# Kernel optimization log

Hardware: AMD Instinct MI355X
Metric: run time of the kernel (lower is better)

The kernel has to match this reference:

```python
import jax, jax.numpy as jnp
import numpy as np

B, L, D = 32, 1024, 1024
H = 8            # hard-coded in FourierBlock weights1 leading dim
E = D // H       # 128
M = 64           # number of retained low-frequency modes
K = 25           # moving_avg kernel (stride 1)
PAD = (K - 1) // 2


def setup_inputs() -> dict:
    key = jax.random.key(0)
    ks = jax.random.split(key, 7)
    scale = 1.0 / (D * D)
    return {
        "x":   jax.random.normal(ks[0], (B, L, D), jnp.float32),
        "Wq":  jax.random.normal(ks[1], (D, D), jnp.float32) * 0.02,
        "bq":  jax.random.normal(ks[2], (D,), jnp.float32) * 0.02,
        "w1r": jax.random.uniform(ks[3], (H, E, E, M), jnp.float32) * scale,
        "w1i": jax.random.uniform(ks[4], (H, E, E, M), jnp.float32) * scale,
        "Wo":  jax.random.normal(ks[5], (D, D), jnp.float32) * 0.02,
        "bo":  jax.random.normal(ks[6], (D,), jnp.float32) * 0.02,
    }


def _forward(x, Wq, bq, w1r, w1i, Wo, bo):
    # --- AutoCorrelationLayer query projection (k,v projections are dead code in FourierBlock) ---
    q = (x @ Wq + bq).reshape(B, L, H, E)          # [B,L,H,E]
    # --- FourierBlock ---
    xq = q.transpose(0, 2, 3, 1)                   # [B,H,E,L]
    x_ft = jnp.fft.rfft(xq, axis=-1)               # [B,H,E,F], F=L//2+1, complex64
    w = w1r + 1j * w1i                             # [H,E,E,M]
    # mode_select='low': index = [0..M-1], output slot wi == i
    out_sel = jnp.einsum("bhem,heom->bhom", x_ft[..., :M], w)   # [B,H,E,M]
    F = L // 2 + 1
    out_ft = jnp.zeros((B, H, E, F), dtype=x_ft.dtype).at[..., :M].set(out_sel)
    y = jnp.fft.irfft(out_ft, n=L, axis=-1)        # [B,H,E,L] real
    # faithful to torch: .view(B, L, -1) on contiguous (B,H,E,L) = flat C-order reshape
    out = y.reshape(B, L, H * E)
    new_x = out @ Wo + bo                          # out_projection
    x2 = x + new_x                                 # dropout is identity in eval
    # --- series_decomp (moving average k=25, replicate padding, stride 1) ---
    xp = jnp.concatenate(
        [jnp.repeat(x2[:, :1], PAD, axis=1), x2, jnp.repeat(x2[:, -1:], PAD, axis=1)],
        axis=1)                                    # [B, L+2*PAD, D]
    cs = jnp.cumsum(xp, axis=1)
    cs = jnp.concatenate([jnp.zeros_like(cs[:, :1]), cs], axis=1)
    moving_mean = (cs[:, K:] - cs[:, :-K]) / K     # [B,L,D]
    res = x2 - moving_mean
    return res


def reference(x, Wq, bq, w1r, w1i, Wo, bo):
    # module returns (x, attn) with attn=None; we return the array output
    return _forward(x, Wq, bq, w1r, w1i, Wo, bo)
```

## Files before the change

kernel.cpp:

```cpp
#include <hip/hip_runtime.h>
#include <hip/hip_bf16.h>

typedef __bf16 bf16x8 __attribute__((ext_vector_type(8)));
typedef float f32x4 __attribute__((ext_vector_type(4)));
typedef unsigned short u16;
typedef unsigned int u32;
typedef unsigned long long u64;


static __device__ __forceinline__ u16 f2b(float f) {
  u32 u = __builtin_bit_cast(u32, f);
  u32 r = (u + 0x7FFFu + ((u >> 16) & 1u)) >> 16;
  return (u16)r;
}
static __device__ __forceinline__ float b2f(u16 s) {
  u32 u = ((u32)s) << 16;
  return __builtin_bit_cast(float, u);
}
static __device__ __forceinline__ u32 pk2(float lo, float hi) {
  return (u32)f2b(lo) | ((u32)f2b(hi) << 16);
}
static __device__ __forceinline__ f32x4 mfma16(bf16x8 a, bf16x8 b, f32x4 c) {
  return __builtin_amdgcn_mfma_f32_16x16x32_bf16(a, b, c, 0, 0, 0);
}

__global__ __launch_bounds__(256) void k_prep(
    const float* __restrict__ Wq, const float* __restrict__ Wo,
    u16* __restrict__ FT, u16* __restrict__ FI2,
    u16* __restrict__ Wq16, u16* __restrict__ Wo16) {
  int idx = blockIdx.x * 256 + threadIdx.x;
  const float W0 = 6.283185307179586f / 1024.0f;
  if (idx < 131072) {
    int m2 = idx >> 10, l = idx & 1023;
    int m = (m2 < 64) ? m2 : (m2 - 64);
    int t = (m * l) & 1023;
    float s, c;
    __sincosf((float)t * W0, &s, &c);
    FT[idx] = f2b((m2 < 64) ? c : -s);
  } else if (idx < 262144) {
    int jj = idx - 131072;
    int j = jj >> 10, l = jj & 1023;
    int m = j >> 1;
    int t = (m * l) & 1023;
    float s, c;
    __sincosf((float)t * W0, &s, &c);
    float v;
    if ((j & 1) == 0) v = (m == 0) ? (1.0f / 1024.0f) : c * (2.0f / 1024.0f);
    else              v = (m == 0) ? 0.0f : -s * (2.0f / 1024.0f);
    FI2[jj] = f2b(v);
  } else if (idx < 262144 + 1048576) {
    int k = idx - 262144;
    Wq16[k] = f2b(Wq[k]);
  } else {
    int k = idx - 1310720;
    Wo16[k] = f2b(Wo[k]);
  }
}

__global__ __launch_bounds__(256) void k_wtrans(
    const float* __restrict__ w1r, const float* __restrict__ w1i,
    u16* __restrict__ W2r, u16* __restrict__ W2i) {
  __shared__ float T[128 * 65];
  int h = blockIdx.x >> 7, e = blockIdx.x & 127;
  int tid = threadIdx.x;
  for (int pass = 0; pass < 2; ++pass) {
    const float* src = pass ? w1i : w1r;
    u16* dst = pass ? W2i : W2r;
    {
      int m = tid & 63, og = tid >> 6;
      const float* sp = src + (((size_t)h * 128 + e) * 128) * 64 + m;
      for (int k = 0; k < 32; ++k) {
        int o = og * 32 + k;
        T[o * 65 + m] = sp[(size_t)o * 64];
      }
    }
    __syncthreads();
    {
      int o = tid & 127, mg = tid >> 7;
      for (int k = 0; k < 32; ++k) {
        int m = mg * 32 + k;
        dst[(((size_t)h * 64 + m) * 128 + e) * 128 + o] = f2b(T[o * 65 + m]);
      }
    }
    __syncthreads();
  }
}

template <int KSTEPS, bool BIAS>
static __device__ __forceinline__ void gemm128(
    const u16* __restrict__ A, size_t arow0, int astride,
    const u16* __restrict__ Bm, int bcol0,
    u16* __restrict__ C, size_t crow0, const float* __restrict__ bias) {
  __shared__ __align__(16) u16 Al[128 * 40];
  __shared__ __align__(16) u16 Bl[128 * 40];
  int tid = threadIdx.x, lane = tid & 63, w = tid >> 6;
  f32x4 acc[2][8];
#pragma unroll
  for (int i = 0; i < 2; i++)
#pragma unroll
    for (int j = 0; j < 8; j++) acc[i][j] = (f32x4){0.f, 0.f, 0.f, 0.f};
  int ar = tid >> 1, ahalf = tid & 1;
  int dloc = tid & 127, lg = tid >> 7;
  for (int kk = 0; kk < KSTEPS; ++kk) {
    {
      const uint4* src = (const uint4*)(A + (arow0 + ar) * (size_t)astride + kk * 32 + ahalf * 16);
      uint4 v0 = src[0], v1 = src[1];
      uint4* dst = (uint4*)(Al + ar * 40 + ahalf * 16);
      dst[0] = v0; dst[1] = v1;
    }
    {
#pragma unroll
      for (int jj = 0; jj < 4; ++jj) {
        int l0 = lg * 16 + jj * 4;
        const u16* bp = Bm + (size_t)(kk * 32 + l0) * 1024 + bcol0 + dloc;
        u16 s0 = bp[0], s1 = bp[1024], s2 = bp[2048], s3 = bp[3072];
        *(u64*)(Bl + dloc * 40 + l0) =
            (u64)s0 | ((u64)s1 << 16) | ((u64)s2 << 32) | ((u64)s3 << 48);
      }
    }
    __syncthreads();
    bf16x8 af[2];
#pragma unroll
    for (int mi = 0; mi < 2; mi++)
      af[mi] = *(const bf16x8*)(Al + (w * 32 + mi * 16 + (lane & 15)) * 40 + 8 * (lane >> 4));
#pragma unroll
    for (int ni = 0; ni < 8; ni++) {
      bf16x8 bf = *(const bf16x8*)(Bl + (ni * 16 + (lane & 15)) * 40 + 8 * (lane >> 4));
#pragma unroll
      for (int mi = 0; mi < 2; mi++) acc[mi][ni] = mfma16(af[mi], bf, acc[mi][ni]);
    }
    __syncthreads();
  }
  if (BIAS) {
    if (w == 0 && (lane >> 4) == 0) {
#pragma unroll
      for (int ni = 0; ni < 8; ni++)
        acc[0][ni][0] += 1024.0f * bias[bcol0 + ni * 16 + (lane & 15)];
    }
  }
#pragma unroll
  for (int mi = 0; mi < 2; mi++)
#pragma unroll
    for (int ni = 0; ni < 8; ni++)
#pragma unroll
      for (int r = 0; r < 4; r++) {
        int row = w * 32 + mi * 16 + 4 * (lane >> 4) + r;
        int col = bcol0 + ni * 16 + (lane & 15);
        C[(crow0 + row) * (size_t)1024 + col] = f2b(acc[mi][ni][r]);
      }
}

__global__ __launch_bounds__(256) void k_dft(const float* __restrict__ x,
                                             const u16* __restrict__ FT,
                                             u16* __restrict__ Z) {
  __shared__ __align__(16) u16 Al[128 * 40];
  __shared__ __align__(16) u16 Bl[128 * 40];
  int b = blockIdx.x >> 3, ct = blockIdx.x & 7;
  int tid = threadIdx.x, lane = tid & 63, w = tid >> 6;
  f32x4 acc[2][8];
#pragma unroll
  for (int i = 0; i < 2; i++)
#pragma unroll
    for (int j = 0; j < 8; j++) acc[i][j] = (f32x4){0.f, 0.f, 0.f, 0.f};
  int am2 = tid >> 1, ahalf = tid & 1;
  int c = tid & 127, lg = tid >> 7;
  for (int kk = 0; kk < 32; ++kk) {
    {
      const uint4* src = (const uint4*)(FT + am2 * 1024 + kk * 32 + ahalf * 16);
      uint4 v0 = src[0], v1 = src[1];
      uint4* dst = (uint4*)(Al + am2 * 40 + ahalf * 16);
      dst[0] = v0; dst[1] = v1;
    }
    {
      const float* xb = x + ((size_t)b * 1024 + kk * 32) * 1024 + ct * 128 + c;
#pragma unroll
      for (int jj = 0; jj < 4; ++jj) {
        int l0 = lg * 16 + jj * 4;
        float f0 = xb[(size_t)(l0 + 0) * 1024];
        float f1 = xb[(size_t)(l0 + 1) * 1024];
        float f2_ = xb[(size_t)(l0 + 2) * 1024];
        float f3 = xb[(size_t)(l0 + 3) * 1024];
        uint2 p = {pk2(f0, f1), pk2(f2_, f3)};
        *(uint2*)(Bl + c * 40 + l0) = p;
      }
    }
    __syncthreads();
    bf16x8 af[2];
#pragma unroll
    for (int mi = 0; mi < 2; mi++)
      af[mi] = *(const bf16x8*)(Al + (w * 32 + mi * 16 + (lane & 15)) * 40 + 8 * (lane >> 4));
#pragma unroll
    for (int ni = 0; ni < 8; ni++) {
      bf16x8 bf = *(const bf16x8*)(Bl + (ni * 16 + (lane & 15)) * 40 + 8 * (lane >> 4));
#pragma unroll
      for (int mi = 0; mi < 2; mi++) acc[mi][ni] = mfma16(af[mi], bf, acc[mi][ni]);
    }
    __syncthreads();
  }
#pragma unroll
  for (int mi = 0; mi < 2; mi++)
#pragma unroll
    for (int ni = 0; ni < 8; ni++)
#pragma unroll
      for (int r = 0; r < 4; r++) {
        int row = w * 32 + mi * 16 + 4 * (lane >> 4) + r;
        int col = ct * 128 + ni * 16 + (lane & 15);
        Z[((size_t)b * 128 + row) * 1024 + col] = f2b(acc[mi][ni][r]);
      }
}

__global__ __launch_bounds__(256) void k_wqmix(const u16* __restrict__ Zm,
                                               const u16* __restrict__ Wq16,
                                               const float* __restrict__ bq,
                                               u16* __restrict__ XF) {
  int mt = blockIdx.x >> 3, nt = blockIdx.x & 7;
  gemm128<32, true>(Zm, (size_t)mt * 128, 1024, Wq16, nt * 128, XF, (size_t)mt * 128, bq);
}

__global__ __launch_bounds__(256) void k_gmat(const u16* __restrict__ FI2,
                                              const u16* __restrict__ Wo16,
                                              u16* __restrict__ G2) {
  int nt = blockIdx.x;
  gemm128<32, false>(FI2, 0, 1024, Wo16, nt * 128, G2, 0, nullptr);
}

__global__ __launch_bounds__(256) void k_modemix(const u16* __restrict__ XF,
                                                 const u16* __restrict__ W2r,
                                                 const u16* __restrict__ W2i,
                                                 u16* __restrict__ OS2T) {
  __shared__ __align__(16) u16 XAr[32 * 200], XAi[32 * 200];
  __shared__ __align__(16) u16 Wbr[128 * 40], Wbi[128 * 40];
  int h = blockIdx.x >> 6, m = blockIdx.x & 63;
  int tid = threadIdx.x, lane = tid & 63, w = tid >> 6;
  {
    int bb = tid >> 3, seg = tid & 7;
    int e0 = seg * 16, kc = seg >> 1, off = (seg & 1) * 16;
    const uint4* sr = (const uint4*)(XF + ((size_t)bb * 128 + m) * 1024 + h * 128 + e0);
    const uint4* si = (const uint4*)(XF + ((size_t)bb * 128 + 64 + m) * 1024 + h * 128 + e0);
    uint4* dr = (uint4*)(XAr + bb * 200 + kc * 40 + off);
    uint4* di = (uint4*)(XAi + bb * 200 + kc * 40 + off);
    dr[0] = sr[0]; dr[1] = sr[1];
    di[0] = si[0]; di[1] = si[1];
  }
  f32x4 accR[2][2], accI[2][2];
#pragma unroll
  for (int i = 0; i < 2; i++)
#pragma unroll
    for (int j = 0; j < 2; j++) {
      accR[i][j] = (f32x4){0.f, 0.f, 0.f, 0.f};
      accI[i][j] = (f32x4){0.f, 0.f, 0.f, 0.f};
    }
  for (int kk = 0; kk < 4; ++kk) {
    {
      int o = tid & 127, pr = tid >> 7;
      const u16* src = (pr ? W2i : W2r) + (((size_t)h * 64 + m) * 128 + kk * 32) * 128 + o;
      u16* dst = (pr ? Wbi : Wbr) + o * 40;
#pragma unroll
      for (int jj = 0; jj < 8; ++jj) {
        int e0 = jj * 4;
        u16 s0 = src[(size_t)(e0 + 0) * 128], s1 = src[(size_t)(e0 + 1) * 128];
        u16 s2 = src[(size_t)(e0 + 2) * 128], s3 = src[(size_t)(e0 + 3) * 128];
        *(u64*)(dst + e0) = (u64)s0 | ((u64)s1 << 16) | ((u64)s2 << 32) | ((u64)s3 << 48);
      }
    }
    __syncthreads();
    bf16x8 ar[2], ai_[2], ain[2];
#pragma unroll
    for (int mi = 0; mi < 2; mi++) {
      int bb = mi * 16 + (lane & 15);
      ar[mi] = *(const bf16x8*)(XAr + bb * 200 + kk * 40 + 8 * (lane >> 4));
      ai_[mi] = *(const bf16x8*)(XAi + bb * 200 + kk * 40 + 8 * (lane >> 4));
      u32 t4[4];
      __builtin_memcpy(t4, &ai_[mi], 16);
#pragma unroll
      for (int q = 0; q < 4; q++) t4[q] ^= 0x80008000u;
      __builtin_memcpy(&ain[mi], t4, 16);
    }
#pragma unroll
    for (int ni = 0; ni < 2; ni++) {
      int o = w * 32 + ni * 16 + (lane & 15);
      bf16x8 br = *(const bf16x8*)(Wbr + o * 40 + 8 * (lane >> 4));
      bf16x8 bi = *(const bf16x8*)(Wbi + o * 40 + 8 * (lane >> 4));
#pragma unroll
      for (int mi = 0; mi < 2; mi++) {
        accR[mi][ni] = mfma16(ar[mi], br, accR[mi][ni]);
        accR[mi][ni] = mfma16(ain[mi], bi, accR[mi][ni]);
        accI[mi][ni] = mfma16(ar[mi], bi, accI[mi][ni]);
        accI[mi][ni] = mfma16(ai_[mi], br, accI[mi][ni]);
      }
    }
    __syncthreads();
  }
#pragma unroll
  for (int mi = 0; mi < 2; mi++)
#pragma unroll
    for (int ni = 0; ni < 2; ni++)
#pragma unroll
      for (int rr = 0; rr < 4; rr++) {
        int brow = mi * 16 + 4 * (lane >> 4) + rr;
        int o = w * 32 + ni * 16 + (lane & 15);
        size_t base = (size_t)brow * 131072 + (size_t)(h * 128 + o) * 128;
        *(u32*)(OS2T + base + 2 * m) = pk2(accR[mi][ni][rr], accI[mi][ni][rr]);
      }
}

__global__ __launch_bounds__(256) void k_nxdecomp(const float* __restrict__ x,
                                                  const u16* __restrict__ OS2T,
                                                  const u16* __restrict__ G2,
                                                  float* __restrict__ out) {
  __shared__ __align__(16) u16 SMEM[160 * 136 + 64 * 136];
  u16* Al = SMEM;
  u16* Bl = SMEM + 160 * 136;
  float* ZT = (float*)SMEM;
  int bid = blockIdx.x;
  int rt = bid & 7, dt = (bid >> 3) & 15, b = bid >> 7;
  int r0 = rt * 128, d0 = dt * 64;
  int tid = threadIdx.x, lane = tid & 63, w = tid >> 6;
  int wr = w >> 1, wc = w & 1;
  for (int it = 0; it < 10; ++it) {
    int q = tid + it * 256;
    int row = q >> 4, seg = q & 15;
    int gr = r0 - 16 + row;
    gr = gr < 0 ? 0 : (gr > 1023 ? 1023 : gr);
    *(uint4*)(Al + row * 136 + seg * 8) =
        *(const uint4*)(OS2T + ((size_t)b * 1024 + gr) * 128 + seg * 8);
  }
  {
    int c = tid & 63, lg = tid >> 6;
#pragma unroll
    for (int jj = 0; jj < 8; ++jj) {
      int l0 = lg * 32 + jj * 4;
      const u16* gp = G2 + (size_t)l0 * 1024 + d0 + c;
      u16 s0 = gp[0], s1 = gp[1024], s2 = gp[2048], s3 = gp[3072];
      *(u64*)(Bl + c * 136 + l0) =
          (u64)s0 | ((u64)s1 << 16) | ((u64)s2 << 32) | ((u64)s3 << 48);
    }
  }
  float xv[5][2][4];
#pragma unroll
  for (int mi = 0; mi < 5; ++mi)
#pragma unroll
    for (int r = 0; r < 4; ++r) {
      int row = wr * 80 + mi * 16 + 4 * (lane >> 4) + r;
      int gr = r0 - 16 + row;
      gr = gr < 0 ? 0 : (gr > 1023 ? 1023 : gr);
#pragma unroll
      for (int ni = 0; ni < 2; ++ni) {
        int col = wc * 32 + ni * 16 + (lane & 15);
        xv[mi][ni][r] = x[((size_t)b * 1024 + gr) * 1024 + d0 + col];
      }
    }
  f32x4 acc[5][2];
#pragma unroll
  for (int i = 0; i < 5; i++)
#pragma unroll
    for (int j = 0; j < 2; j++) acc[i][j] = (f32x4){0.f, 0.f, 0.f, 0.f};
  __syncthreads();
#pragma unroll
  for (int kk = 0; kk < 4; ++kk) {
    bf16x8 af[5], bf[2];
#pragma unroll
    for (int mi = 0; mi < 5; ++mi)
      af[mi] = *(const bf16x8*)(Al + (wr * 80 + mi * 16 + (lane & 15)) * 136 +
                                kk * 32 + 8 * (lane >> 4));
#pragma unroll
    for (int ni = 0; ni < 2; ++ni)
      bf[ni] = *(const bf16x8*)(Bl + (wc * 32 + ni * 16 + (lane & 15)) * 136 +
                                kk * 32 + 8 * (lane >> 4));
#pragma unroll
    for (int mi = 0; mi < 5; ++mi)
#pragma unroll
      for (int ni = 0; ni < 2; ++ni) acc[mi][ni] = mfma16(af[mi], bf[ni], acc[mi][ni]);
  }
  __syncthreads();
#pragma unroll
  for (int mi = 0; mi < 5; ++mi)
#pragma unroll
    for (int ni = 0; ni < 2; ++ni)
#pragma unroll
      for (int r = 0; r < 4; ++r) {
        int row = wr * 80 + mi * 16 + 4 * (lane >> 4) + r;
        int col = wc * 32 + ni * 16 + (lane & 15);
        ZT[row * 68 + col] = acc[mi][ni][r] + xv[mi][ni][r];
      }
  __syncthreads();
  {
    int c = tid & 63, h2 = tid >> 6;
    int j0 = h2 * 32;
    float s = 0.f;
#pragma unroll
    for (int u = 0; u < 25; ++u) s += ZT[(j0 + 4 + u) * 68 + c];
    for (int j = j0; j < j0 + 32; ++j) {
      float center = ZT[(j + 16) * 68 + c];
      out[((size_t)b * 1024 + r0 + j) * 1024 + d0 + c] = center - s * (1.0f / 25.0f);
      if (j < j0 + 31) s += ZT[(j + 29) * 68 + c] - ZT[(j + 4) * 68 + c];
    }
  }
}

extern "C" void kernel_launch(void* const* d_in, const int* in_sizes, int n_in,
                              void* d_out, int out_size, void* d_ws, size_t ws_size,
                              hipStream_t stream) {
  const float* x = (const float*)d_in[0];
  const float* Wq = (const float*)d_in[1];
  const float* bq = (const float*)d_in[2];
  const float* w1r = (const float*)d_in[3];
  const float* w1i = (const float*)d_in[4];
  const float* Wo = (const float*)d_in[5];

  char* ws = (char*)d_ws;
  u16* FT = (u16*)(ws + 0x000000);
  u16* FI2 = (u16*)(ws + 0x040000);
  u16* Wq16 = (u16*)(ws + 0x080000);
  u16* Wo16 = (u16*)(ws + 0x280000);
  u16* G2 = (u16*)(ws + 0x480000);
  u16* OS2T = (u16*)(ws + 0x4C0000);

  char* ob = (char*)d_out;
  u16* W2r = (u16*)(ob + 0x0000000);
  u16* W2i = (u16*)(ob + 0x1000000);
  u16* Zm = (u16*)(ob + 0x2000000);
  u16* XF = (u16*)(ob + 0x2800000);

  k_prep<<<9216, 256, 0, stream>>>(Wq, Wo, FT, FI2, Wq16, Wo16);
  k_wtrans<<<1024, 256, 0, stream>>>(w1r, w1i, W2r, W2i);
  k_gmat<<<8, 256, 0, stream>>>(FI2, Wo16, G2);
  k_dft<<<256, 256, 0, stream>>>(x, FT, Zm);
  k_wqmix<<<256, 256, 0, stream>>>(Zm, Wq16, bq, XF);
  k_modemix<<<512, 256, 0, stream>>>(XF, W2r, W2i, OS2T);
  k_nxdecomp<<<4096, 256, 0, stream>>>(x, OS2T, G2, (float*)d_out);
}
```

Measured before the change: 429.4 us.

## Register-prefetch next K-tile in GEMMs and load MFMA fragments directly from global

The shared GEMM helper and the DFT kernel now prefetch the next K-step's A and B tiles into registers before the MFMAs of the current step, so global load latency overlaps compute. The mode-mixing kernel keeps its X fragments in registers instead of LDS and prefetches weight slices. The G matrix is stored transposed, which lets the final decomposition kernel read MFMA operands straight from global memory with its own register double buffering and drop the LDS staging for A and B. The cost is higher register pressure, which may lower occupancy, and uncoalesced transposed stores in the small gmat kernel.

```diff
diff --git a/kernel.cpp b/kernel.cpp
--- a/kernel.cpp
+++ b/kernel.cpp
@@ -12,10 +12,6 @@
   u32 u = __builtin_bit_cast(u32, f);
   u32 r = (u + 0x7FFFu + ((u >> 16) & 1u)) >> 16;
   return (u16)r;
-}
-static __device__ __forceinline__ float b2f(u16 s) {
-  u32 u = ((u32)s) << 16;
-  return __builtin_bit_cast(float, u);
 }
 static __device__ __forceinline__ u32 pk2(float lo, float hi) {
   return (u32)f2b(lo) | ((u32)f2b(hi) << 16);
@@ -86,8 +82,8 @@
   }
 }
 
-template <int KSTEPS, bool BIAS>
-static __device__ __forceinline__ void gemm128(
+template <int KSTEPS, bool BIAS, bool TSTORE>
+static __device__ __forceinline__ void gemm128_db(
     const u16* __restrict__ A, size_t arow0, int astride,
     const u16* __restrict__ Bm, int bcol0,
     u16* __restrict__ C, size_t crow0, const float* __restrict__ bias) {
@@ -101,24 +97,42 @@
     for (int j = 0; j < 8; j++) acc[i][j] = (f32x4){0.f, 0.f, 0.f, 0.f};
   int ar = tid >> 1, ahalf = tid & 1;
   int dloc = tid & 127, lg = tid >> 7;
+  const u16* aptr = A + (arow0 + ar) * (size_t)astride + ahalf * 16;
+  const u16* bptr = Bm + (size_t)(lg * 16) * 1024 + bcol0 + dloc;
+  uint4 av0, av1;
+  u16 bs[16];
+  av0 = *(const uint4*)aptr;
+  av1 = *(const uint4*)(aptr + 8);
+#pragma unroll
+  for (int jj = 0; jj < 4; ++jj) {
+    const u16* bp = bptr + (size_t)(jj * 4) * 1024;
+    bs[jj * 4 + 0] = bp[0]; bs[jj * 4 + 1] = bp[1024];
+    bs[jj * 4 + 2] = bp[2048]; bs[jj * 4 + 3] = bp[3072];
+  }
   for (int kk = 0; kk < KSTEPS; ++kk) {
     {
-      const uint4* src = (const uint4*)(A + (arow0 + ar) * (size_t)astride + kk * 32 + ahalf * 16);
-      uint4 v0 = src[0], v1 = src[1];
       uint4* dst = (uint4*)(Al + ar * 40 + ahalf * 16);
-      dst[0] = v0; dst[1] = v1;
-    }
-    {
+      dst[0] = av0; dst[1] = av1;
+    }
+#pragma unroll
+    for (int jj = 0; jj < 4; ++jj) {
+      int l0 = lg * 16 + jj * 4;
+      *(u64*)(Bl + dloc * 40 + l0) = (u64)bs[jj * 4] | ((u64)bs[jj * 4 + 1] << 16) |
+                                     ((u64)bs[jj * 4 + 2] << 32) | ((u64)bs[jj * 4 + 3] << 48);
+    }
+    __syncthreads();
+    if (kk + 1 < KSTEPS) {
+      const u16* ap = aptr + (kk + 1) * 32;
+      av0 = *(const uint4*)ap;
+      av1 = *(const uint4*)(ap + 8);
+      const u16* bk = bptr + (size_t)((kk + 1) * 32) * 1024;
 #pragma unroll
       for (int jj = 0; jj < 4; ++jj) {
-        int l0 = lg * 16 + jj * 4;
-        const u16* bp = Bm + (size_t)(kk * 32 + l0) * 1024 + bcol0 + dloc;
-        u16 s0 = bp[0], s1 = bp[1024], s2 = bp[2048], s3 = bp[3072];
-        *(u64*)(Bl + dloc * 40 + l0) =
-            (u64)s0 | ((u64)s1 << 16) | ((u64)s2 << 32) | ((u64)s3 << 48);
-      }
-    }
-    __syncthreads();
+        const u16* bp = bk + (size_t)(jj * 4) * 1024;
+        bs[jj * 4 + 0] = bp[0]; bs[jj * 4 + 1] = bp[1024];
+        bs[jj * 4 + 2] = bp[2048]; bs[jj * 4 + 3] = bp[3072];
+      }
+    }
     bf16x8 af[2];
 #pragma unroll
     for (int mi = 0; mi < 2; mi++)
@@ -138,16 +152,29 @@
         acc[0][ni][0] += 1024.0f * bias[bcol0 + ni * 16 + (lane & 15)];
     }
   }
-#pragma unroll
-  for (int mi = 0; mi < 2; mi++)
-#pragma unroll
-    for (int ni = 0; ni < 8; ni++)
-#pragma unroll
-      for (int r = 0; r < 4; r++) {
-        int row = w * 32 + mi * 16 + 4 * (lane >> 4) + r;
+  if (TSTORE) {
+#pragma unroll
+    for (int mi = 0; mi < 2; mi++)
+#pragma unroll
+      for (int ni = 0; ni < 8; ni++) {
+        int row0 = w * 32 + mi * 16 + 4 * (lane >> 4);
         int col = bcol0 + ni * 16 + (lane & 15);
-        C[(crow0 + row) * (size_t)1024 + col] = f2b(acc[mi][ni][r]);
-      }
+        u64 pk = (u64)f2b(acc[mi][ni][0]) | ((u64)f2b(acc[mi][ni][1]) << 16) |
+                 ((u64)f2b(acc[mi][ni][2]) << 32) | ((u64)f2b(acc[mi][ni][3]) << 48);
+        *(u64*)(C + (size_t)col * 128 + row0) = pk;
+      }
+  } else {
+#pragma unroll
+    for (int mi = 0; mi < 2; mi++)
+#pragma unroll
+      for (int ni = 0; ni < 8; ni++)
+#pragma unroll
+        for (int r = 0; r < 4; r++) {
+          int row = w * 32 + mi * 16 + 4 * (lane >> 4) + r;
+          int col = bcol0 + ni * 16 + (lane & 15);
+          C[(crow0 + row) * (size_t)1024 + col] = f2b(acc[mi][ni][r]);
+        }
+  }
 }
 
 __global__ __launch_bounds__(256) void k_dft(const float* __restrict__ x,
@@ -162,29 +189,43 @@
   for (int i = 0; i < 2; i++)
 #pragma unroll
     for (int j = 0; j < 8; j++) acc[i][j] = (f32x4){0.f, 0.f, 0.f, 0.f};
-  int am2 = tid >> 1, ahalf = tid & 1;
+  int ar = tid >> 1, ahalf = tid & 1;
   int c = tid & 127, lg = tid >> 7;
+  const u16* aptr = FT + ar * 1024 + ahalf * 16;
+  const float* bbase = x + ((size_t)b * 1024) * 1024 + ct * 128 + c;
+  uint4 av0, av1;
+  float bx[16];
+  av0 = *(const uint4*)aptr;
+  av1 = *(const uint4*)(aptr + 8);
+#pragma unroll
+  for (int jj = 0; jj < 4; ++jj) {
+    const float* bp = bbase + (size_t)(lg * 16 + jj * 4) * 1024;
+    bx[jj * 4 + 0] = bp[0]; bx[jj * 4 + 1] = bp[1024];
+    bx[jj * 4 + 2] = bp[2048]; bx[jj * 4 + 3] = bp[3072];
+  }
   for (int kk = 0; kk < 32; ++kk) {
     {
-      const uint4* src = (const uint4*)(FT + am2 * 1024 + kk * 32 + ahalf * 16);
-      uint4 v0 = src[0], v1 = src[1];
-      uint4* dst = (uint4*)(Al + am2 * 40 + ahalf * 16);
-      dst[0] = v0; dst[1] = v1;
-    }
-    {
-      const float* xb = x + ((size_t)b * 1024 + kk * 32) * 1024 + ct * 128 + c;
+      uint4* dst = (uint4*)(Al + ar * 40 + ahalf * 16);
+      dst[0] = av0; dst[1] = av1;
+    }
+#pragma unroll
+    for (int jj = 0; jj < 4; ++jj) {
+      uint2 p = {pk2(bx[jj * 4], bx[jj * 4 + 1]), pk2(bx[jj * 4 + 2], bx[jj * 4 + 3])};
+      *(uint2*)(Bl + c * 40 + lg * 16 + jj * 4) = p;
+    }
+    __syncthreads();
+    if (kk < 31) {
+      const u16* ap = aptr + (kk + 1) * 32;
+      av0 = *(const uint4*)ap;
+      av1 = *(const uint4*)(ap + 8);
+      const float* bk = bbase + (size_t)((kk + 1) * 32) * 1024;
 #pragma unroll
       for (int jj = 0; jj < 4; ++jj) {
-        int l0 = lg * 16 + jj * 4;
-        float f0 = xb[(size_t)(l0 + 0) * 1024];
-        float f1 = xb[(size_t)(l0 + 1) * 1024];
-        float f2_ = xb[(size_t)(l0 + 2) * 1024];
-        float f3 = xb[(size_t)(l0 + 3) * 1024];
-        uint2 p = {pk2(f0, f1), pk2(f2_, f3)};
-        *(uint2*)(Bl + c * 40 + l0) = p;
-      }
-    }
-    __syncthreads();
+        const float* bp = bk + (size_t)(jj * 4) * 1024;
+        bx[jj * 4 + 0] = bp[0]; bx[jj * 4 + 1] = bp[1024];
+        bx[jj * 4 + 2] = bp[2048]; bx[jj * 4 + 3] = bp[3072];
+      }
+    }
     bf16x8 af[2];
 #pragma unroll
     for (int mi = 0; mi < 2; mi++)
@@ -214,34 +255,41 @@
                                                const float* __restrict__ bq,
                                                u16* __restrict__ XF) {
   int mt = blockIdx.x >> 3, nt = blockIdx.x & 7;
-  gemm128<32, true>(Zm, (size_t)mt * 128, 1024, Wq16, nt * 128, XF, (size_t)mt * 128, bq);
+  gemm128_db<32, true, false>(Zm, (size_t)mt * 128, 1024, Wq16, nt * 128, XF,
+                              (size_t)mt * 128, bq);
 }
 
 __global__ __launch_bounds__(256) void k_gmat(const u16* __restrict__ FI2,
                                               const u16* __restrict__ Wo16,
-                                              u16* __restrict__ G2) {
+                                              u16* __restrict__ G2T) {
   int nt = blockIdx.x;
-  gemm128<32, false>(FI2, 0, 1024, Wo16, nt * 128, G2, 0, nullptr);
+  gemm128_db<32, false, true>(FI2, 0, 1024, Wo16, nt * 128, G2T, 0, nullptr);
 }
 
 __global__ __launch_bounds__(256) void k_modemix(const u16* __restrict__ XF,
                                                  const u16* __restrict__ W2r,
                                                  const u16* __restrict__ W2i,
                                                  u16* __restrict__ OS2T) {
-  __shared__ __align__(16) u16 XAr[32 * 200], XAi[32 * 200];
   __shared__ __align__(16) u16 Wbr[128 * 40], Wbi[128 * 40];
   int h = blockIdx.x >> 6, m = blockIdx.x & 63;
   int tid = threadIdx.x, lane = tid & 63, w = tid >> 6;
-  {
-    int bb = tid >> 3, seg = tid & 7;
-    int e0 = seg * 16, kc = seg >> 1, off = (seg & 1) * 16;
-    const uint4* sr = (const uint4*)(XF + ((size_t)bb * 128 + m) * 1024 + h * 128 + e0);
-    const uint4* si = (const uint4*)(XF + ((size_t)bb * 128 + 64 + m) * 1024 + h * 128 + e0);
-    uint4* dr = (uint4*)(XAr + bb * 200 + kc * 40 + off);
-    uint4* di = (uint4*)(XAi + bb * 200 + kc * 40 + off);
-    dr[0] = sr[0]; dr[1] = sr[1];
-    di[0] = si[0]; di[1] = si[1];
-  }
+  bf16x8 xar[2][4], xai[2][4];
+#pragma unroll
+  for (int mi = 0; mi < 2; ++mi) {
+    int bb = mi * 16 + (lane & 15);
+    const u16* xr = XF + ((size_t)(bb * 128 + m)) * 1024 + h * 128 + 8 * (lane >> 4);
+    const u16* xi = XF + ((size_t)(bb * 128 + 64 + m)) * 1024 + h * 128 + 8 * (lane >> 4);
+#pragma unroll
+    for (int kk = 0; kk < 4; ++kk) {
+      xar[mi][kk] = *(const bf16x8*)(xr + kk * 32);
+      xai[mi][kk] = *(const bf16x8*)(xi + kk * 32);
+    }
+  }
+  int o = tid & 127, pr = tid >> 7;
+  const u16* wsrc = (pr ? W2i : W2r) + ((size_t)(h * 64 + m) * 128) * 128 + o;
+  u16 ws_[32];
+#pragma unroll
+  for (int e = 0; e < 32; ++e) ws_[e] = wsrc[(size_t)e * 128];
   f32x4 accR[2][2], accI[2][2];
 #pragma unroll
   for (int i = 0; i < 2; i++)
@@ -252,41 +300,38 @@
     }
   for (int kk = 0; kk < 4; ++kk) {
     {
-      int o = tid & 127, pr = tid >> 7;
-      const u16* src = (pr ? W2i : W2r) + (((size_t)h * 64 + m) * 128 + kk * 32) * 128 + o;
-      u16* dst = (pr ? Wbi : Wbr) + o * 40;
-#pragma unroll
-      for (int jj = 0; jj < 8; ++jj) {
-        int e0 = jj * 4;
-        u16 s0 = src[(size_t)(e0 + 0) * 128], s1 = src[(size_t)(e0 + 1) * 128];
-        u16 s2 = src[(size_t)(e0 + 2) * 128], s3 = src[(size_t)(e0 + 3) * 128];
-        *(u64*)(dst + e0) = (u64)s0 | ((u64)s1 << 16) | ((u64)s2 << 32) | ((u64)s3 << 48);
-      }
-    }
-    __syncthreads();
-    bf16x8 ar[2], ai_[2], ain[2];
+      u16* wdst = (pr ? Wbi : Wbr) + o * 40;
+#pragma unroll
+      for (int jj = 0; jj < 8; ++jj)
+        *(u64*)(wdst + jj * 4) = (u64)ws_[jj * 4] | ((u64)ws_[jj * 4 + 1] << 16) |
+                                 ((u64)ws_[jj * 4 + 2] << 32) | ((u64)ws_[jj * 4 + 3] << 48);
+    }
+    __syncthreads();
+    if (kk < 3) {
+      const u16* wk = wsrc + (size_t)((kk + 1) * 32) * 128;
+#pragma unroll
+      for (int e = 0; e < 32; ++e) ws_[e] = wk[(size_t)e * 128];
+    }
+    bf16x8 ain[2];
 #pragma unroll
     for (int mi = 0; mi < 2; mi++) {
-      int bb = mi * 16 + (lane & 15);
-      ar[mi] = *(const bf16x8*)(XAr + bb * 200 + kk * 40 + 8 * (lane >> 4));
-      ai_[mi] = *(const bf16x8*)(XAi + bb * 200 + kk * 40 + 8 * (lane >> 4));
       u32 t4[4];
-      __builtin_memcpy(t4, &ai_[mi], 16);
+      __builtin_memcpy(t4, &xai[mi][kk], 16);
 #pragma unroll
       for (int q = 0; q < 4; q++) t4[q] ^= 0x80008000u;
       __builtin_memcpy(&ain[mi], t4, 16);
     }
 #pragma unroll
     for (int ni = 0; ni < 2; ni++) {
-      int o = w * 32 + ni * 16 + (lane & 15);
-      bf16x8 br = *(const bf16x8*)(Wbr + o * 40 + 8 * (lane >> 4));
-      bf16x8 bi = *(const bf16x8*)(Wbi + o * 40 + 8 * (lane >> 4));
+      int o2 = w * 32 + ni * 16 + (lane & 15);
+      bf16x8 br = *(const bf16x8*)(Wbr + o2 * 40 + 8 * (lane >> 4));
+      bf16x8 bi = *(const bf16x8*)(Wbi + o2 * 40 + 8 * (lane >> 4));
 #pragma unroll
       for (int mi = 0; mi < 2; mi++) {
-        accR[mi][ni] = mfma16(ar[mi], br, accR[mi][ni]);
+        accR[mi][ni] = mfma16(xar[mi][kk], br, accR[mi][ni]);
         accR[mi][ni] = mfma16(ain[mi], bi, accR[mi][ni]);
-        accI[mi][ni] = mfma16(ar[mi], bi, accI[mi][ni]);
-        accI[mi][ni] = mfma16(ai_[mi], br, accI[mi][ni]);
+        accI[mi][ni] = mfma16(xar[mi][kk], bi, accI[mi][ni]);
+        accI[mi][ni] = mfma16(xai[mi][kk], br, accI[mi][ni]);
       }
     }
     __syncthreads();
@@ -298,45 +343,65 @@
 #pragma unroll
       for (int rr = 0; rr < 4; rr++) {
         int brow = mi * 16 + 4 * (lane >> 4) + rr;
-        int o = w * 32 + ni * 16 + (lane & 15);
-        size_t base = (size_t)brow * 131072 + (size_t)(h * 128 + o) * 128;
+        int o3 = w * 32 + ni * 16 + (lane & 15);
+        size_t base = (size_t)brow * 131072 + (size_t)(h * 128 + o3) * 128;
         *(u32*)(OS2T + base + 2 * m) = pk2(accR[mi][ni][rr], accI[mi][ni][rr]);
       }
 }
 
 __global__ __launch_bounds__(256) void k_nxdecomp(const float* __restrict__ x,
                                                   const u16* __restrict__ OS2T,
-                                                  const u16* __restrict__ G2,
+                                                  const u16* __restrict__ G2T,
                                                   float* __restrict__ out) {
-  __shared__ __align__(16) u16 SMEM[160 * 136 + 64 * 136];
-  u16* Al = SMEM;
-  u16* Bl = SMEM + 160 * 136;
-  float* ZT = (float*)SMEM;
+  __shared__ float ZT[160 * 68];
   int bid = blockIdx.x;
   int rt = bid & 7, dt = (bid >> 3) & 15, b = bid >> 7;
   int r0 = rt * 128, d0 = dt * 64;
   int tid = threadIdx.x, lane = tid & 63, w = tid >> 6;
   int wr = w >> 1, wc = w & 1;
-  for (int it = 0; it < 10; ++it) {
-    int q = tid + it * 256;
-    int row = q >> 4, seg = q & 15;
+  const u16* pA[5];
+#pragma unroll
+  for (int mi = 0; mi < 5; ++mi) {
+    int row = wr * 80 + mi * 16 + (lane & 15);
     int gr = r0 - 16 + row;
     gr = gr < 0 ? 0 : (gr > 1023 ? 1023 : gr);
-    *(uint4*)(Al + row * 136 + seg * 8) =
-        *(const uint4*)(OS2T + ((size_t)b * 1024 + gr) * 128 + seg * 8);
-  }
-  {
-    int c = tid & 63, lg = tid >> 6;
-#pragma unroll
-    for (int jj = 0; jj < 8; ++jj) {
-      int l0 = lg * 32 + jj * 4;
-      const u16* gp = G2 + (size_t)l0 * 1024 + d0 + c;
-      u16 s0 = gp[0], s1 = gp[1024], s2 = gp[2048], s3 = gp[3072];
-      *(u64*)(Bl + c * 136 + l0) =
-          (u64)s0 | ((u64)s1 << 16) | ((u64)s2 << 32) | ((u64)s3 << 48);
-    }
-  }
-  float xv[5][2][4];
+    pA[mi] = OS2T + ((size_t)b * 1024 + gr) * 128 + 8 * (lane >> 4);
+  }
+  const u16* pB[2];
+#pragma unroll
+  for (int ni = 0; ni < 2; ++ni) {
+    int col = d0 + wc * 32 + ni * 16 + (lane & 15);
+    pB[ni] = G2T + (size_t)col * 128 + 8 * (lane >> 4);
+  }
+  f32x4 acc[5][2];
+#pragma unroll
+  for (int i = 0; i < 5; i++)
+#pragma unroll
+    for (int j = 0; j < 2; j++) acc[i][j] = (f32x4){0.f, 0.f, 0.f, 0.f};
+  bf16x8 aC[5], bC[2], aN[5], bN[2];
+#pragma unroll
+  for (int i = 0; i < 5; ++i) aC[i] = *(const bf16x8*)(pA[i]);
+#pragma unroll
+  for (int i = 0; i < 2; ++i) bC[i] = *(const bf16x8*)(pB[i]);
+#pragma unroll
+  for (int kk = 0; kk < 4; ++kk) {
+    if (kk < 3) {
+#pragma unroll
+      for (int i = 0; i < 5; ++i) aN[i] = *(const bf16x8*)(pA[i] + (kk + 1) * 32);
+#pragma unroll
+      for (int i = 0; i < 2; ++i) bN[i] = *(const bf16x8*)(pB[i] + (kk + 1) * 32);
+    }
+#pragma unroll
+    for (int mi = 0; mi < 5; ++mi)
+#pragma unroll
+      for (int ni = 0; ni < 2; ++ni) acc[mi][ni] = mfma16(aC[mi], bC[ni], acc[mi][ni]);
+    if (kk < 3) {
+#pragma unroll
+      for (int i = 0; i < 5; ++i) aC[i] = aN[i];
+#pragma unroll
+      for (int i = 0; i < 2; ++i) bC[i] = bN[i];
+    }
+  }
 #pragma unroll
   for (int mi = 0; mi < 5; ++mi)
 #pragma unroll
@@ -344,45 +409,13 @@
       int row = wr * 80 + mi * 16 + 4 * (lane >> 4) + r;
       int gr = r0 - 16 + row;
       gr = gr < 0 ? 0 : (gr > 1023 ? 1023 : gr);
+      const float* xp = x + ((size_t)b * 1024 + gr) * 1024 + d0;
 #pragma unroll
       for (int ni = 0; ni < 2; ++ni) {
         int col = wc * 32 + ni * 16 + (lane & 15);
-        xv[mi][ni][r] = x[((size_t)b * 1024 + gr) * 1024 + d0 + col];
-      }
-    }
-  f32x4 acc[5][2];
-#pragma unroll
-  for (int i = 0; i < 5; i++)
-#pragma unroll
-    for (int j = 0; j < 2; j++) acc[i][j] = (f32x4){0.f, 0.f, 0.f, 0.f};
-  __syncthreads();
-#pragma unroll
-  for (int kk = 0; kk < 4; ++kk) {
-    bf16x8 af[5], bf[2];
-#pragma unroll
-    for (int mi = 0; mi < 5; ++mi)
-      af[mi] = *(const bf16x8*)(Al + (wr * 80 + mi * 16 + (lane & 15)) * 136 +
-                                kk * 32 + 8 * (lane >> 4));
-#pragma unroll
-    for (int ni = 0; ni < 2; ++ni)
-      bf[ni] = *(const bf16x8*)(Bl + (wc * 32 + ni * 16 + (lane & 15)) * 136 +
-                                kk * 32 + 8 * (lane >> 4));
-#pragma unroll
-    for (int mi = 0; mi < 5; ++mi)
-#pragma unroll
-      for (int ni = 0; ni < 2; ++ni) acc[mi][ni] = mfma16(af[mi], bf[ni], acc[mi][ni]);
-  }
-  __syncthreads();
-#pragma unroll
-  for (int mi = 0; mi < 5; ++mi)
-#pragma unroll
-    for (int ni = 0; ni < 2; ++ni)
-#pragma unroll
-      for (int r = 0; r < 4; ++r) {
-        int row = wr * 80 + mi * 16 + 4 * (lane >> 4) + r;
-        int col = wc * 32 + ni * 16 + (lane & 15);
-        ZT[row * 68 + col] = acc[mi][ni][r] + xv[mi][ni][r];
-      }
+        ZT[row * 68 + col] = acc[mi][ni][r] + xp[col];
+      }
+    }
   __syncthreads();
   {
     int c = tid & 63, h2 = tid >> 6;
@@ -413,7 +446,7 @@
   u16* FI2 = (u16*)(ws + 0x040000);
   u16* Wq16 = (u16*)(ws + 0x080000);
   u16* Wo16 = (u16*)(ws + 0x280000);
-  u16* G2 = (u16*)(ws + 0x480000);
+  u16* G2T = (u16*)(ws + 0x480000);
   u16* OS2T = (u16*)(ws + 0x4C0000);
 
   char* ob = (char*)d_out;
@@ -424,9 +457,9 @@
 
   k_prep<<<9216, 256, 0, stream>>>(Wq, Wo, FT, FI2, Wq16, Wo16);
   k_wtrans<<<1024, 256, 0, stream>>>(w1r, w1i, W2r, W2i);
-  k_gmat<<<8, 256, 0, stream>>>(FI2, Wo16, G2);
+  k_gmat<<<8, 256, 0, stream>>>(FI2, Wo16, G2T);
   k_dft<<<256, 256, 0, stream>>>(x, FT, Zm);
   k_wqmix<<<256, 256, 0, stream>>>(Zm, Wq16, bq, XF);
   k_modemix<<<512, 256, 0, stream>>>(XF, W2r, W2i, OS2T);
-  k_nxdecomp<<<4096, 256, 0, stream>>>(x, OS2T, G2, (float*)d_out);
-}
+  k_nxdecomp<<<4096, 256, 0, stream>>>(x, OS2T, G2T, (float*)d_out);
+}
```

Result: no change. 435.9 us (+1.5%).
